# Performance work log

Measured on AMD Instinct MI355X. Metric: run time of the kernel, lower is better.

## Reference

```python
import math
import jax, jax.numpy as jnp
import numpy as np

B, S, D = 2, 2048, 4096
H, KVH = 32, 8
HD = D // H            # 128
REP = H // KVH         # 4


def setup_inputs() -> dict:
    key = jax.random.key(0)
    ks = jax.random.split(key, 7)
    scale = 1.0 / math.sqrt(D)
    return {
        "x": jax.random.normal(ks[0], (B, S, D), dtype=jnp.float32),
        "freqs_cos": jax.random.uniform(ks[1], (S, HD // 2), dtype=jnp.float32),
        "freqs_sin": jax.random.uniform(ks[2], (S, HD // 2), dtype=jnp.float32),
        "Wq": jax.random.normal(ks[3], (D, H * HD), dtype=jnp.float32) * scale,
        "Wk": jax.random.normal(ks[4], (D, KVH * HD), dtype=jnp.float32) * scale,
        "Wv": jax.random.normal(ks[5], (D, KVH * HD), dtype=jnp.float32) * scale,
        "Wo": jax.random.normal(ks[6], (H * HD, D), dtype=jnp.float32) * scale,
    }


def _rope(t, cos, sin):
    # t: [B,S,h,HD]; pairs are interleaved (reshape to (HD//2, 2) in original)
    tr = t[..., 0::2]
    ti = t[..., 1::2]
    cos = cos[None, :, None, :]  # [1,S,1,HD//2]
    sin = sin[None, :, None, :]
    out_r = tr * cos - ti * sin
    out_i = tr * sin + ti * cos
    return jnp.stack([out_r, out_i], axis=-1).reshape(t.shape)


def reference(x, freqs_cos, freqs_sin, Wq, Wk, Wv, Wo):
    b, s, _ = x.shape
    xq = (x @ Wq).reshape(b, s, H, HD)
    xk = (x @ Wk).reshape(b, s, KVH, HD)
    xv = (x @ Wv).reshape(b, s, KVH, HD)

    xq = _rope(xq, freqs_cos, freqs_sin)
    xk = _rope(xk, freqs_cos, freqs_sin)

    # GQA: repeat each kv head REP times -> [b,s,H,HD]
    xk = jnp.repeat(xk, REP, axis=2)
    xv = jnp.repeat(xv, REP, axis=2)

    q = xq.transpose(0, 2, 1, 3)  # [b,H,s,HD]
    k = xk.transpose(0, 2, 1, 3)
    v = xv.transpose(0, 2, 1, 3)

    scores = jnp.einsum('bhqd,bhkd->bhqk', q, k) / math.sqrt(HD)
    causal = jnp.tril(jnp.ones((s, s), dtype=bool))
    scores = jnp.where(causal[None, None], scores, jnp.float32(-jnp.inf))
    probs = jax.nn.softmax(scores.astype(jnp.float32), axis=-1).astype(x.dtype)

    out = jnp.einsum('bhqk,bhkd->bhqd', probs, v)
    out = out.transpose(0, 2, 1, 3).reshape(b, s, H * HD)
    return out @ Wo
```

## Files before the change

### kernel.cpp

```cpp
#include <hip/hip_runtime.h>

typedef unsigned short u16;
typedef unsigned int u32;
typedef __attribute__((ext_vector_type(8))) short bf16x8;
typedef __attribute__((ext_vector_type(8))) unsigned short u16x8;
typedef __attribute__((ext_vector_type(4))) unsigned short u16x4;
typedef __attribute__((ext_vector_type(4))) float f32x4;
typedef __attribute__((ext_vector_type(4))) unsigned int u32x4;

#define S_LEN 2048
#define NB 2
#define NH 32
#define NKVH 8
#define HD 128
#define DMODEL 4096
#define NEG_BIG (-1.0e30f)

__device__ __forceinline__ float bf2f(u16 x) {
  union { u32 u; float f; } v; v.u = ((u32)x) << 16; return v.f;
}
__device__ __forceinline__ u16 f2bf(float f) {
  union { float f; u32 u; } v; v.f = f;
  u32 r = v.u + 0x7FFFu + ((v.u >> 16) & 1u);
  return (u16)(r >> 16);
}

__device__ __forceinline__ void gload16(const void* g, void* l) {
  __builtin_amdgcn_global_load_lds(
      (const __attribute__((address_space(1))) void*)g,
      (__attribute__((address_space(3))) void*)l, 16, 0, 0);
}

__global__ __launch_bounds__(256) void convert_x(const float* __restrict__ x,
                                                 u16* __restrict__ xb)
{
  int i = blockIdx.x * 256 + threadIdx.x;
  f32x4 a = *(const f32x4*)&x[(size_t)i * 8];
  f32x4 b = *(const f32x4*)&x[(size_t)i * 8 + 4];
  u16x8 h = { f2bf(a[0]), f2bf(a[1]), f2bf(a[2]), f2bf(a[3]),
              f2bf(b[0]), f2bf(b[1]), f2bf(b[2]), f2bf(b[3]) };
  *(u16x8*)&xb[(size_t)i * 8] = h;
}

__global__ __launch_bounds__(256) void transpose_w(const float* __restrict__ W,
                                                   u16* __restrict__ out,
                                                   int N)
{
  __shared__ u16 Ls[64 * 68];
  const int t  = threadIdx.x;
  const int k0 = blockIdx.x * 64;
  const int n0 = blockIdx.y * 64;
#pragma unroll
  for (int i = 0; i < 4; ++i) {
    int kr = (t >> 4) + i * 16;
    int nc = (t & 15) * 4;
    f32x4 v = *(const f32x4*)&W[(size_t)(k0 + kr) * N + n0 + nc];
    u16x4 h = { f2bf(v[0]), f2bf(v[1]), f2bf(v[2]), f2bf(v[3]) };
    *(u16x4*)&Ls[kr * 68 + nc] = h;
  }
  __syncthreads();
#pragma unroll
  for (int i = 0; i < 2; ++i) {
    int nr = (t >> 3) + i * 32;
    int kc = (t & 7) * 8;
    u16x8 h;
#pragma unroll
    for (int j = 0; j < 8; ++j) h[j] = Ls[(kc + j) * 68 + nr];
    *(u16x8*)&out[(size_t)(n0 + nr) * 4096 + k0 + kc] = h;
  }
}

__global__ __launch_bounds__(256) void transpose_v(const u16* __restrict__ Yv,
                                                   u16* __restrict__ Vt)
{
  __shared__ u16 Ls[64 * 68];
  const int t  = threadIdx.x;
  const int s0 = blockIdx.x * 64;
  const int d0 = blockIdx.y * 64;
  const int z  = blockIdx.z;
#pragma unroll
  for (int i = 0; i < 2; ++i) {
    int sr = (t >> 3) + i * 32;
    int dc = (t & 7) * 8;
    u16x8 v = *(const u16x8*)&Yv[((size_t)(z >> 3) * S_LEN + s0 + sr) * 1024 +
                                 (z & 7) * 128 + d0 + dc];
    u16x4 lo = { v[0], v[1], v[2], v[3] };
    u16x4 hi = { v[4], v[5], v[6], v[7] };
    *(u16x4*)&Ls[sr * 68 + dc]     = lo;
    *(u16x4*)&Ls[sr * 68 + dc + 4] = hi;
  }
  __syncthreads();
#pragma unroll
  for (int i = 0; i < 2; ++i) {
    int dr = (t >> 3) + i * 32;
    int sc = (t & 7) * 8;
    u16x8 h;
#pragma unroll
    for (int j = 0; j < 8; ++j) h[j] = Ls[(sc + j) * 68 + dr];
    *(u16x8*)&Vt[((size_t)z * 128 + d0 + dr) * S_LEN + s0 + sc] = h;
  }
}

__global__ __launch_bounds__(256) void gemm_qkv(const u16* __restrict__ A,
                                                const u16* __restrict__ Bt,
                                                u16* __restrict__ Yq,
                                                u16* __restrict__ Yk,
                                                u16* __restrict__ Yv)
{
  __shared__ u16 As[128 * 64];
  __shared__ u16 Bs[128 * 64];
  const int tid  = threadIdx.x;
  const int wave = tid >> 6;
  const int lane = tid & 63;
  const int lr   = lane & 15;
  const int quad = lane >> 4;
  const int wm   = (wave >> 1) * 64;
  const int wn   = (wave & 1) * 64;
  const int bm   = blockIdx.y * 128;
  const int bn   = blockIdx.x * 128;

  const int col = (lane & 7) * 8;
  const int r0  = wave * 32 + (lane >> 3);

  const f32x4 zero = {0.f, 0.f, 0.f, 0.f};
  f32x4 acc[4][4];
#pragma unroll
  for (int i = 0; i < 4; ++i)
#pragma unroll
    for (int j = 0; j < 4; ++j) acc[i][j] = zero;

  for (int kt = 0; kt < 4096; kt += 64) {
    __syncthreads();
#pragma unroll
    for (int c = 0; c < 4; ++c) {
      gload16(&A [(size_t)(bm + r0 + c * 8) * 4096 + kt + col],
              &As[wave * 2048 + c * 512]);
      gload16(&Bt[(size_t)(bn + r0 + c * 8) * 4096 + kt + col],
              &Bs[wave * 2048 + c * 512]);
    }
    __syncthreads();

#pragma unroll
    for (int kk = 0; kk < 2; ++kk) {
      bf16x8 af[4], bfr[4];
#pragma unroll
      for (int mt = 0; mt < 4; ++mt)
        af[mt] = *(const bf16x8*)&As[(wm + mt * 16 + lr) * 64 + kk * 32 + quad * 8];
#pragma unroll
      for (int nt = 0; nt < 4; ++nt)
        bfr[nt] = *(const bf16x8*)&Bs[(wn + nt * 16 + lr) * 64 + kk * 32 + quad * 8];
#pragma unroll
      for (int mt = 0; mt < 4; ++mt)
#pragma unroll
        for (int nt = 0; nt < 4; ++nt)
          acc[mt][nt] = __builtin_amdgcn_mfma_f32_16x16x32_bf16(af[mt], bfr[nt], acc[mt][nt], 0, 0, 0);
    }
  }

  u16* dst; size_t ldc; int nbase;
  if (bn < 4096)      { dst = Yq; ldc = 4096; nbase = bn; }
  else if (bn < 5120) { dst = Yk; ldc = 1024; nbase = bn - 4096; }
  else                { dst = Yv; ldc = 1024; nbase = bn - 5120; }
#pragma unroll
  for (int mt = 0; mt < 4; ++mt)
#pragma unroll
    for (int nt = 0; nt < 4; ++nt)
#pragma unroll
      for (int r = 0; r < 4; ++r) {
        size_t m = (size_t)(bm + wm + mt * 16 + quad * 4 + r);
        size_t n = (size_t)(nbase + wn + nt * 16 + lr);
        dst[m * ldc + n] = f2bf(acc[mt][nt][r]);
      }
}

__global__ __launch_bounds__(256) void gemm_o(const u16* __restrict__ A,
                                              const u16* __restrict__ Bt,
                                              float* __restrict__ C)
{
  __shared__ u16 As[128 * 64];
  __shared__ u16 Bs[128 * 64];
  const int tid  = threadIdx.x;
  const int wave = tid >> 6;
  const int lane = tid & 63;
  const int lr   = lane & 15;
  const int quad = lane >> 4;
  const int wm   = (wave >> 1) * 64;
  const int wn   = (wave & 1) * 64;
  const int bm   = blockIdx.y * 128;
  const int bn   = blockIdx.x * 128;

  const int col = (lane & 7) * 8;
  const int r0  = wave * 32 + (lane >> 3);

  const f32x4 zero = {0.f, 0.f, 0.f, 0.f};
  f32x4 acc[4][4];
#pragma unroll
  for (int i = 0; i < 4; ++i)
#pragma unroll
    for (int j = 0; j < 4; ++j) acc[i][j] = zero;

  for (int kt = 0; kt < 4096; kt += 64) {
    __syncthreads();
#pragma unroll
    for (int c = 0; c < 4; ++c) {
      gload16(&A [(size_t)(bm + r0 + c * 8) * 4096 + kt + col],
              &As[wave * 2048 + c * 512]);
      gload16(&Bt[(size_t)(bn + r0 + c * 8) * 4096 + kt + col],
              &Bs[wave * 2048 + c * 512]);
    }
    __syncthreads();

#pragma unroll
    for (int kk = 0; kk < 2; ++kk) {
      bf16x8 af[4], bfr[4];
#pragma unroll
      for (int mt = 0; mt < 4; ++mt)
        af[mt] = *(const bf16x8*)&As[(wm + mt * 16 + lr) * 64 + kk * 32 + quad * 8];
#pragma unroll
      for (int nt = 0; nt < 4; ++nt)
        bfr[nt] = *(const bf16x8*)&Bs[(wn + nt * 16 + lr) * 64 + kk * 32 + quad * 8];
#pragma unroll
      for (int mt = 0; mt < 4; ++mt)
#pragma unroll
        for (int nt = 0; nt < 4; ++nt)
          acc[mt][nt] = __builtin_amdgcn_mfma_f32_16x16x32_bf16(af[mt], bfr[nt], acc[mt][nt], 0, 0, 0);
    }
  }

#pragma unroll
  for (int mt = 0; mt < 4; ++mt)
#pragma unroll
    for (int nt = 0; nt < 4; ++nt)
#pragma unroll
      for (int r = 0; r < 4; ++r) {
        size_t m = (size_t)(bm + wm + mt * 16 + quad * 4 + r);
        size_t n = (size_t)(bn + wn + nt * 16 + lr);
        C[m * 4096 + n] = acc[mt][nt][r];
      }
}

__global__ __launch_bounds__(256) void rope_v(u16* __restrict__ Y,
                                              const float* __restrict__ cp,
                                              const float* __restrict__ sp,
                                              int log2nh, int total)
{
  int g = blockIdx.x * 256 + threadIdx.x;
  if (g >= total) return;
  int j = (g & 15) * 4;
  int s = (g >> (4 + log2nh)) & (S_LEN - 1);
  u16x8 t = *(const u16x8*)&Y[(size_t)g * 8];
  f32x4 c  = *(const f32x4*)&cp[s * 64 + j];
  f32x4 sn = *(const f32x4*)&sp[s * 64 + j];
  u16x8 o;
#pragma unroll
  for (int p = 0; p < 4; ++p) {
    float tr = bf2f(t[2 * p]);
    float ti = bf2f(t[2 * p + 1]);
    o[2 * p]     = f2bf(tr * c[p] - ti * sn[p]);
    o[2 * p + 1] = f2bf(tr * sn[p] + ti * c[p]);
  }
  *(u16x8*)&Y[(size_t)g * 8] = o;
}

__global__ __launch_bounds__(256) void attn_kernel(const u16* Q,
                                                   const u16* __restrict__ K,
                                                   const u16* __restrict__ V,
                                                   u16* O)
{
  __shared__ u16 Ks[64 * 136];
  __shared__ u16 Vs[128 * 72];
  __shared__ u16 Ps[4 * 16 * 72];

  const int tid  = threadIdx.x;
  const int wave = tid >> 6;
  const int lane = tid & 63;
  const int lr   = lane & 15;
  const int quad = lane >> 4;

  const int b   = blockIdx.z;
  const int h   = blockIdx.y;
  const int q0  = ((int)gridDim.x - 1 - (int)blockIdx.x) * 64;
  const int kvh = h >> 2;

  const int qrow = q0 + wave * 16 + lr;
  const u16* qptr = Q + ((size_t)((b * S_LEN + qrow) * NH + h)) * HD;
  bf16x8 aq[4];
#pragma unroll
  for (int c = 0; c < 4; ++c) aq[c] = *(const bf16x8*)(qptr + c * 32 + quad * 8);

  const f32x4 zero = {0.f, 0.f, 0.f, 0.f};
  f32x4 accO[8];
#pragma unroll
  for (int nt = 0; nt < 8; ++nt) accO[nt] = zero;
  float m_run[4], l_run[4];
#pragma unroll
  for (int r = 0; r < 4; ++r) { m_run[r] = NEG_BIG; l_run[r] = 0.f; }

  const float scale = 0.08838834764831845f;
  const int myq = q0 + wave * 16 + quad * 4;

  int krow_[4], d0_[4], vd_[4], vk8_[4];
  size_t kbase[4], vbase[4];
#pragma unroll
  for (int i = 0; i < 4; ++i) {
    int e = (tid + i * 256) * 8;
    krow_[i] = e >> 7;
    d0_[i]   = e & 127;
    int cch = tid + i * 256;
    vd_[i]  = cch >> 3;
    vk8_[i] = cch & 7;
    kbase[i] = ((size_t)((b * S_LEN + krow_[i]) * NKVH + kvh)) * HD + d0_[i];
    vbase[i] = ((size_t)((b * NKVH + kvh) * HD + vd_[i])) * S_LEN + vk8_[i] * 8;
  }

  u32x4 kreg[4], vreg[4];
#pragma unroll
  for (int i = 0; i < 4; ++i) {
    kreg[i] = *(const u32x4*)&K[kbase[i]];
    vreg[i] = *(const u32x4*)&V[vbase[i]];
  }

  for (int kv0 = 0; kv0 <= q0; kv0 += 64) {
    const bool diag = (kv0 == q0);
    __syncthreads();
#pragma unroll
    for (int i = 0; i < 4; ++i) {
      *(u32x4*)&Ks[krow_[i] * 136 + d0_[i]] = kreg[i];
      *(u32x4*)&Vs[vd_[i] * 72 + ((vk8_[i] * 8) ^ (((vd_[i] >> 3) & 7) << 3))] = vreg[i];
    }
    __syncthreads();

    if (kv0 + 64 <= q0) {
#pragma unroll
      for (int i = 0; i < 4; ++i) {
        kreg[i] = *(const u32x4*)&K[kbase[i] + (size_t)(kv0 + 64) * (NKVH * HD)];
        vreg[i] = *(const u32x4*)&V[vbase[i] + kv0 + 64];
      }
    }

    f32x4 sa[4];
#pragma unroll
    for (int t = 0; t < 4; ++t) {
      f32x4 a = zero;
#pragma unroll
      for (int c = 0; c < 4; ++c) {
        bf16x8 bk = *(const bf16x8*)&Ks[(t * 16 + lr) * 136 + c * 32 + quad * 8];
        a = __builtin_amdgcn_mfma_f32_16x16x32_bf16(aq[c], bk, a, 0, 0, 0);
      }
      sa[t] = a;
    }

    float alpha[4];
#pragma unroll
    for (int r = 0; r < 4; ++r) {
      const int row = myq + r;
      float s[4];
#pragma unroll
      for (int t = 0; t < 4; ++t) {
        float v = sa[t][r] * scale;
        if (diag) v = (kv0 + t * 16 + lr <= row) ? v : NEG_BIG;
        s[t] = v;
      }
      float mx = fmaxf(fmaxf(s[0], s[1]), fmaxf(s[2], s[3]));
#pragma unroll
      for (int off = 8; off >= 1; off >>= 1) mx = fmaxf(mx, __shfl_xor(mx, off));
      float mn = fmaxf(m_run[r], mx);
      alpha[r] = __expf(m_run[r] - mn);
      m_run[r] = mn;
      float p[4], rs = 0.f;
#pragma unroll
      for (int t = 0; t < 4; ++t) { p[t] = __expf(s[t] - mn); rs += p[t]; }
#pragma unroll
      for (int off = 8; off >= 1; off >>= 1) rs += __shfl_xor(rs, off);
      l_run[r] = l_run[r] * alpha[r] + rs;
      const int q  = quad * 4 + r;
      const int sw = (q & 7) << 3;
      const int base = wave * 1152 + q * 72;
#pragma unroll
      for (int t = 0; t < 4; ++t) Ps[base + ((t * 16 + lr) ^ sw)] = f2bf(p[t]);
    }
#pragma unroll
    for (int nt = 0; nt < 8; ++nt)
#pragma unroll
      for (int r = 0; r < 4; ++r) accO[nt][r] *= alpha[r];

#pragma unroll
    for (int kt2 = 0; kt2 < 2; ++kt2) {
      bf16x8 pf = *(const bf16x8*)&Ps[wave * 1152 + lr * 72 +
                                      ((kt2 * 32 + quad * 8) ^ ((lr & 7) << 3))];
#pragma unroll
      for (int nt = 0; nt < 8; ++nt) {
        const int d = nt * 16 + lr;
        bf16x8 vf = *(const bf16x8*)&Vs[d * 72 +
                                        ((kt2 * 32 + quad * 8) ^ (((d >> 3) & 7) << 3))];
        accO[nt] = __builtin_amdgcn_mfma_f32_16x16x32_bf16(pf, vf, accO[nt], 0, 0, 0);
      }
    }
  }

  float rl[4];
#pragma unroll
  for (int r = 0; r < 4; ++r) rl[r] = 1.0f / l_run[r];
#pragma unroll
  for (int nt = 0; nt < 8; ++nt)
#pragma unroll
    for (int r = 0; r < 4; ++r) {
      size_t q = (size_t)(q0 + wave * 16 + quad * 4 + r);
      O[((size_t)b * S_LEN + q) * DMODEL + (size_t)h * HD + nt * 16 + lr] =
          f2bf(accO[nt][r] * rl[r]);
    }
}

extern "C" void kernel_launch(void* const* d_in, const int* in_sizes, int n_in,
                              void* d_out, int out_size, void* d_ws, size_t ws_size,
                              hipStream_t stream)
{
  const float* x  = (const float*)d_in[0];
  const float* cp = (const float*)d_in[1];
  const float* sp = (const float*)d_in[2];
  const float* Wq = (const float*)d_in[3];
  const float* Wk = (const float*)d_in[4];
  const float* Wv = (const float*)d_in[5];
  const float* Wo = (const float*)d_in[6];

  u16* Wt  = (u16*)d_ws;
  u16* Yq  = Wt + (size_t)25165824;
  u16* Yk  = Yq + (size_t)16777216;
  u16* Yv  = Yk + (size_t)4194304;
  u16* att = Yq;
  u16* WoT = Wt;
  u16* Vt  = Wt;
  u16* xb  = (u16*)d_out;

  transpose_w<<<dim3(64, 64), 256, 0, stream>>>(Wq, Wt,                    4096);
  transpose_w<<<dim3(64, 16), 256, 0, stream>>>(Wk, Wt + (size_t)4096*4096, 1024);
  transpose_w<<<dim3(64, 16), 256, 0, stream>>>(Wv, Wt + (size_t)5120*4096, 1024);
  convert_x<<<8192, 256, 0, stream>>>(x, xb);
  gemm_qkv<<<dim3(48, 32), 256, 0, stream>>>(xb, Wt, Yq, Yk, Yv);
  rope_v<<<8192, 256, 0, stream>>>(Yq, cp, sp, 5, 2097152);
  rope_v<<<2048, 256, 0, stream>>>(Yk, cp, sp, 3, 524288);
  transpose_v<<<dim3(32, 2, 16), 256, 0, stream>>>(Yv, Vt);
  attn_kernel<<<dim3(32, 32, 2), 256, 0, stream>>>(Yq, Yk, Vt, att);
  transpose_w<<<dim3(64, 64), 256, 0, stream>>>(Wo, WoT, 4096);
  gemm_o<<<dim3(32, 32), 256, 0, stream>>>(att, WoT, (float*)d_out);
}
```

Measured before the change: 1.070 ms.

## Swizzle GEMM LDS tiles and compute softmax row sums via extra MFMA column

The QKV and output GEMMs now XOR-swizzle the 16-byte chunk index of their shared-memory tiles on both store and load, to remove LDS bank conflicts on the MFMA fragment reads. The attention kernel extends the V tile with a ones column, so that the P·V MFMA also accumulates the softmax denominator. This replaces the per-row exp-sum shuffle reductions, at the cost of one extra MFMA per k-step, extra LDS and accumulator registers, and a sum taken from bf16-rounded probabilities.

```diff
diff --git a/kernel.cpp b/kernel.cpp
--- a/kernel.cpp
+++ b/kernel.cpp
@@ -119,7 +119,7 @@
   const int bm   = blockIdx.y * 128;
   const int bn   = blockIdx.x * 128;
 
-  const int col = (lane & 7) * 8;
+  const int col = (((lane & 7) ^ (lane >> 3)) * 8);
   const int r0  = wave * 32 + (lane >> 3);
 
   const f32x4 zero = {0.f, 0.f, 0.f, 0.f};
@@ -145,10 +145,12 @@
       bf16x8 af[4], bfr[4];
 #pragma unroll
       for (int mt = 0; mt < 4; ++mt)
-        af[mt] = *(const bf16x8*)&As[(wm + mt * 16 + lr) * 64 + kk * 32 + quad * 8];
+        af[mt] = *(const bf16x8*)&As[(wm + mt * 16 + lr) * 64 +
+                                     (((kk * 4 + quad) ^ (lr & 7)) * 8)];
 #pragma unroll
       for (int nt = 0; nt < 4; ++nt)
-        bfr[nt] = *(const bf16x8*)&Bs[(wn + nt * 16 + lr) * 64 + kk * 32 + quad * 8];
+        bfr[nt] = *(const bf16x8*)&Bs[(wn + nt * 16 + lr) * 64 +
+                                      (((kk * 4 + quad) ^ (lr & 7)) * 8)];
 #pragma unroll
       for (int mt = 0; mt < 4; ++mt)
 #pragma unroll
@@ -189,7 +191,7 @@
   const int bm   = blockIdx.y * 128;
   const int bn   = blockIdx.x * 128;
 
-  const int col = (lane & 7) * 8;
+  const int col = (((lane & 7) ^ (lane >> 3)) * 8);
   const int r0  = wave * 32 + (lane >> 3);
 
   const f32x4 zero = {0.f, 0.f, 0.f, 0.f};
@@ -215,10 +217,12 @@
       bf16x8 af[4], bfr[4];
 #pragma unroll
       for (int mt = 0; mt < 4; ++mt)
-        af[mt] = *(const bf16x8*)&As[(wm + mt * 16 + lr) * 64 + kk * 32 + quad * 8];
+        af[mt] = *(const bf16x8*)&As[(wm + mt * 16 + lr) * 64 +
+                                     (((kk * 4 + quad) ^ (lr & 7)) * 8)];
 #pragma unroll
       for (int nt = 0; nt < 4; ++nt)
-        bfr[nt] = *(const bf16x8*)&Bs[(wn + nt * 16 + lr) * 64 + kk * 32 + quad * 8];
+        bfr[nt] = *(const bf16x8*)&Bs[(wn + nt * 16 + lr) * 64 +
+                                      (((kk * 4 + quad) ^ (lr & 7)) * 8)];
 #pragma unroll
       for (int mt = 0; mt < 4; ++mt)
 #pragma unroll
@@ -268,7 +272,7 @@
                                                    u16* O)
 {
   __shared__ u16 Ks[64 * 136];
-  __shared__ u16 Vs[128 * 72];
+  __shared__ u16 Vs[144 * 72];
   __shared__ u16 Ps[4 * 16 * 72];
 
   const int tid  = threadIdx.x;
@@ -282,6 +286,11 @@
   const int q0  = ((int)gridDim.x - 1 - (int)blockIdx.x) * 64;
   const int kvh = h >> 2;
 
+  for (int i = tid; i < 16 * 72; i += 256) {
+    int dd = i / 72;
+    Vs[(size_t)(128 + dd) * 72 + (i % 72)] = (dd == 0) ? (u16)0x3F80 : (u16)0;
+  }
+
   const int qrow = q0 + wave * 16 + lr;
   const u16* qptr = Q + ((size_t)((b * S_LEN + qrow) * NH + h)) * HD;
   bf16x8 aq[4];
@@ -289,12 +298,12 @@
   for (int c = 0; c < 4; ++c) aq[c] = *(const bf16x8*)(qptr + c * 32 + quad * 8);
 
   const f32x4 zero = {0.f, 0.f, 0.f, 0.f};
-  f32x4 accO[8];
-#pragma unroll
-  for (int nt = 0; nt < 8; ++nt) accO[nt] = zero;
-  float m_run[4], l_run[4];
-#pragma unroll
-  for (int r = 0; r < 4; ++r) { m_run[r] = NEG_BIG; l_run[r] = 0.f; }
+  f32x4 accO[9];
+#pragma unroll
+  for (int nt = 0; nt < 9; ++nt) accO[nt] = zero;
+  float m_run[4];
+#pragma unroll
+  for (int r = 0; r < 4; ++r) m_run[r] = NEG_BIG;
 
   const float scale = 0.08838834764831845f;
   const int myq = q0 + wave * 16 + quad * 4;
@@ -367,20 +376,15 @@
       float mn = fmaxf(m_run[r], mx);
       alpha[r] = __expf(m_run[r] - mn);
       m_run[r] = mn;
-      float p[4], rs = 0.f;
-#pragma unroll
-      for (int t = 0; t < 4; ++t) { p[t] = __expf(s[t] - mn); rs += p[t]; }
-#pragma unroll
-      for (int off = 8; off >= 1; off >>= 1) rs += __shfl_xor(rs, off);
-      l_run[r] = l_run[r] * alpha[r] + rs;
       const int q  = quad * 4 + r;
       const int sw = (q & 7) << 3;
       const int base = wave * 1152 + q * 72;
 #pragma unroll
-      for (int t = 0; t < 4; ++t) Ps[base + ((t * 16 + lr) ^ sw)] = f2bf(p[t]);
-    }
-#pragma unroll
-    for (int nt = 0; nt < 8; ++nt)
+      for (int t = 0; t < 4; ++t)
+        Ps[base + ((t * 16 + lr) ^ sw)] = f2bf(__expf(s[t] - mn));
+    }
+#pragma unroll
+    for (int nt = 0; nt < 9; ++nt)
 #pragma unroll
       for (int r = 0; r < 4; ++r) accO[nt][r] *= alpha[r];
 
@@ -389,7 +393,7 @@
       bf16x8 pf = *(const bf16x8*)&Ps[wave * 1152 + lr * 72 +
                                       ((kt2 * 32 + quad * 8) ^ ((lr & 7) << 3))];
 #pragma unroll
-      for (int nt = 0; nt < 8; ++nt) {
+      for (int nt = 0; nt < 9; ++nt) {
         const int d = nt * 16 + lr;
         bf16x8 vf = *(const bf16x8*)&Vs[d * 72 +
                                         ((kt2 * 32 + quad * 8) ^ (((d >> 3) & 7) << 3))];
@@ -400,7 +404,10 @@
 
   float rl[4];
 #pragma unroll
-  for (int r = 0; r < 4; ++r) rl[r] = 1.0f / l_run[r];
+  for (int r = 0; r < 4; ++r) {
+    float l = __shfl(accO[8][r], lane & 48);
+    rl[r] = 1.0f / l;
+  }
 #pragma unroll
   for (int nt = 0; nt < 8; ++nt)
 #pragma unroll
```

After: 951.1 us. 11.1% less time.
